# Kernel optimization log

Measured on AMD Instinct MI355X. Metric: run time of the kernel, lower is better.

## Reference

```python
import jax, jax.numpy as jnp
import numpy as np

D = 1024
H = 16
K = 32768
EPS = 1e-5


def setup_inputs() -> dict:
    key = jax.random.key(0)
    ks = jax.random.split(key, 12)
    s = 1.0 / np.sqrt(D)
    return {
        "query": jax.random.normal(ks[0], (D,), jnp.float32),
        "neighbors": jax.random.normal(ks[1], (K, D), jnp.float32),
        # nn.MultiheadAttention params
        "in_proj_w": jax.random.uniform(ks[2], (3 * D, D), jnp.float32, -s, s),
        "in_proj_b": jnp.zeros((3 * D,), jnp.float32),
        "out_proj_w": jax.random.uniform(ks[3], (D, D), jnp.float32, -s, s),
        "out_proj_b": jnp.zeros((D,), jnp.float32),
        # FFN params
        "w1": jax.random.uniform(ks[4], (4 * D, D), jnp.float32, -s, s),
        "b1": jnp.zeros((4 * D,), jnp.float32),
        "w2": jax.random.uniform(ks[5], (D, 4 * D), jnp.float32, -s, s),
        "b2": jnp.zeros((D,), jnp.float32),
        # LayerNorm params
        "g1": jnp.ones((D,), jnp.float32),
        "be1": jnp.zeros((D,), jnp.float32),
        "g2": jnp.ones((D,), jnp.float32),
        "be2": jnp.zeros((D,), jnp.float32),
    }


def _layernorm(x, g, b):
    m = jnp.mean(x, axis=-1, keepdims=True)
    v = jnp.var(x, axis=-1, keepdims=True)
    return (x - m) * jax.lax.rsqrt(v + EPS) * g + b


def reference(query, neighbors, in_proj_w, in_proj_b, out_proj_w, out_proj_b,
              w1, b1, w2, b2, g1, be1, g2, be2):
    dh = D // H
    wq, wk, wv = in_proj_w[:D], in_proj_w[D:2 * D], in_proj_w[2 * D:]
    bq, bk, bv = in_proj_b[:D], in_proj_b[D:2 * D], in_proj_b[2 * D:]

    q = (query @ wq.T + bq).reshape(H, dh)            # [H, dh]
    k = (neighbors @ wk.T + bk).reshape(K, H, dh)     # [K, H, dh]
    v = (neighbors @ wv.T + bv).reshape(K, H, dh)

    scores = jnp.einsum('hd,khd->hk', q, k) / np.sqrt(dh)  # [H, K]
    attn = jax.nn.softmax(scores, axis=-1)
    ctx = jnp.einsum('hk,khd->hd', attn, v).reshape(D)      # [D]
    attn_out = ctx @ out_proj_w.T + out_proj_b

    x = _layernorm(query + attn_out, g1, be1)
    ffn = jax.nn.gelu(x @ w1.T + b1, approximate=False) @ w2.T + b2
    return _layernorm(x + ffn, g2, be2)
```

## Files before the change

### kernel.cpp

```cpp
#include <hip/hip_runtime.h>
#include <hip/hip_bf16.h>

#define D 1024
#define H 16
#define DH 64
#define KN 32768
#define EPS 1e-5f

__device__ __forceinline__ float wave_sum(float v){
  #pragma unroll
  for (int off = 32; off; off >>= 1) v += __shfl_xor(v, off, 64);
  return v;
}

#define GLL(gp, lp) __builtin_amdgcn_global_load_lds((const __attribute__((address_space(1))) void*)(gp), (__attribute__((address_space(3))) void*)(lp), 16, 0, 0)

__global__ void g_qproj(const float* __restrict__ query, const float* __restrict__ ipw,
                        const float* __restrict__ ipb, float* __restrict__ q){
  int j = blockIdx.x, l = threadIdx.x;
  const float4* qv = (const float4*)(query + l*16);
  const float4* wv = (const float4*)(ipw + (size_t)j*D + l*16);
  float acc = 0.f;
  #pragma unroll
  for (int t = 0; t < 4; t++){
    float4 a = qv[t], b = wv[t];
    acc += a.x*b.x + a.y*b.y + a.z*b.z + a.w*b.w;
  }
  acc = wave_sum(acc);
  if (l == 0) q[j] = acc + ipb[j];
}

__global__ __launch_bounds__(256) void g_qk(const float* __restrict__ ipw, const float* __restrict__ ipb,
                                            const float* __restrict__ q, float* __restrict__ qk,
                                            float* __restrict__ sb){
  int b = blockIdx.x, t = threadIdx.x;
  int h = b >> 2, sl = b & 3;
  int jg = t >> 6, c = t & 63;
  __shared__ float qh[DH];
  __shared__ float4 red[256];
  if (t < DH) qh[t] = q[h*DH + t];
  __syncthreads();
  if (t < DH){
    float p = qh[t] * ipb[D + h*DH + t];
    p = wave_sum(p);
    if (t == 0 && sl == 0) sb[h] = p;
  }
  float4 acc = make_float4(0.f,0.f,0.f,0.f);
  for (int jj = 0; jj < 16; jj++){
    int j = jg*16 + jj;
    float4 w = *((const float4*)(ipw + (size_t)(D + h*DH + j)*D) + sl*64 + c);
    float qj = qh[j];
    acc.x += qj*w.x; acc.y += qj*w.y; acc.z += qj*w.z; acc.w += qj*w.w;
  }
  red[t] = acc;
  __syncthreads();
  if (jg == 0){
    float4 a = red[c], b1 = red[64+c], c1 = red[128+c], d1 = red[192+c];
    float4 r = make_float4(a.x+b1.x+c1.x+d1.x, a.y+b1.y+c1.y+d1.y,
                           a.z+b1.z+c1.z+d1.z, a.w+b1.w+c1.w+d1.w);
    ((float4*)(qk + h*D))[sl*64 + c] = r;
  }
}

__global__ __launch_bounds__(256, 2) void g_attn(const float* __restrict__ nbr, const float* __restrict__ qk,
                       const float* __restrict__ sb, float* __restrict__ lpart,
                       float* __restrict__ part, int rows_per_blk){
  __shared__ __align__(16) float tile[2][8*D];
  const int t = threadIdx.x;
  const int w = t >> 6, ci = t & 63;
  const int wb = t & ~63;
  const int g = (ci >> 4) & 3;
  const float sbl = sb[w*4 + g];

  float qk0[16], qk1[16], qk2[16], qk3[16];
  {
    const float4* p0 = (const float4*)(qk + (w*4+0)*D);
    const float4* p1 = (const float4*)(qk + (w*4+1)*D);
    const float4* p2 = (const float4*)(qk + (w*4+2)*D);
    const float4* p3 = (const float4*)(qk + (w*4+3)*D);
    #pragma unroll
    for (int c = 0; c < 4; c++){
      float4 f;
      f = p0[c*64 + ci]; qk0[4*c]=f.x; qk0[4*c+1]=f.y; qk0[4*c+2]=f.z; qk0[4*c+3]=f.w;
      f = p1[c*64 + ci]; qk1[4*c]=f.x; qk1[4*c+1]=f.y; qk1[4*c+2]=f.z; qk1[4*c+3]=f.w;
      f = p2[c*64 + ci]; qk2[4*c]=f.x; qk2[4*c+1]=f.y; qk2[4*c+2]=f.z; qk2[4*c+3]=f.w;
      f = p3[c*64 + ci]; qk3[4*c]=f.x; qk3[4*c+1]=f.y; qk3[4*c+2]=f.z; qk3[4*c+3]=f.w;
    }
  }
  float acc0[16], acc1[16], acc2[16], acc3[16];
  #pragma unroll
  for (int i = 0; i < 16; i++){ acc0[i]=0.f; acc1[i]=0.f; acc2[i]=0.f; acc3[i]=0.f; }
  float lsum = 0.f;

  const int k0 = blockIdx.x * rows_per_blk;
  const int ntiles = rows_per_blk >> 3;
  const uint4* gb = (const uint4*)nbr;

  {
    const uint4* gsrc = gb + (size_t)k0*256;
    #pragma unroll
    for (int i = 0; i < 8; i++) GLL(gsrc + i*256 + t, &tile[0][(i*256 + wb)*4]);
  }
  __syncthreads();

  #pragma unroll 1
  for (int tl = 0; tl < ntiles; tl++){
    int cur = tl & 1;
    if (tl + 1 < ntiles){
      const uint4* gsrc = gb + (size_t)(k0 + (tl+1)*8)*256;
      #pragma unroll
      for (int i = 0; i < 8; i++) GLL(gsrc + i*256 + t, &tile[cur^1][(i*256 + wb)*4]);
    }
    #pragma unroll 1
    for (int r = 0; r < 8; r++){
      const float4* row4 = (const float4*)(tile[cur]) + r*256;
      float xf[16];
      float s0=0.f, s1=0.f, s2=0.f, s3=0.f;
      #pragma unroll
      for (int c = 0; c < 4; c++){
        float4 a = row4[c*64 + ci];
        xf[4*c]=a.x; xf[4*c+1]=a.y; xf[4*c+2]=a.z; xf[4*c+3]=a.w;
        s0 += a.x*qk0[4*c] + a.y*qk0[4*c+1] + a.z*qk0[4*c+2] + a.w*qk0[4*c+3];
        s1 += a.x*qk1[4*c] + a.y*qk1[4*c+1] + a.z*qk1[4*c+2] + a.w*qk1[4*c+3];
        s2 += a.x*qk2[4*c] + a.y*qk2[4*c+1] + a.z*qk2[4*c+2] + a.w*qk2[4*c+3];
        s3 += a.x*qk3[4*c] + a.y*qk3[4*c+1] + a.z*qk3[4*c+2] + a.w*qk3[4*c+3];
      }
      const bool lo32 = (ci & 32) == 0;
      float za = lo32 ? s2 : s0;
      float ka = lo32 ? s0 : s2;
      float u02 = ka + __shfl_xor(za, 32, 64);
      float zb = lo32 ? s3 : s1;
      float kb = lo32 ? s1 : s3;
      float u13 = kb + __shfl_xor(zb, 32, 64);
      const bool lo16 = (ci & 16) == 0;
      float zc = lo16 ? u13 : u02;
      float kc = lo16 ? u02 : u13;
      float v = kc + __shfl_xor(zc, 16, 64);
      v += __shfl_xor(v, 8, 64);
      v += __shfl_xor(v, 4, 64);
      v += __shfl_xor(v, 2, 64);
      v += __shfl_xor(v, 1, 64);
      float pv = __expf((v + sbl)*0.125f);
      lsum += pv;
      float p0 = __shfl(pv, 0, 64);
      float p1 = __shfl(pv, 16, 64);
      float p2 = __shfl(pv, 32, 64);
      float p3 = __shfl(pv, 48, 64);
      #pragma unroll
      for (int j = 0; j < 16; j++){
        acc0[j] += p0*xf[j];
        acc1[j] += p1*xf[j];
        acc2[j] += p2*xf[j];
        acc3[j] += p3*xf[j];
      }
    }
    __syncthreads();
  }

  if ((ci & 15) == 0) lpart[blockIdx.x*H + w*4 + g] = lsum;
  float4* o = (float4*)(part + (size_t)blockIdx.x*(H*D) + (size_t)(w*4)*D);
  #pragma unroll
  for (int c = 0; c < 4; c++){
    o[0*256 + c*64 + ci] = make_float4(acc0[4*c], acc0[4*c+1], acc0[4*c+2], acc0[4*c+3]);
    o[1*256 + c*64 + ci] = make_float4(acc1[4*c], acc1[4*c+1], acc1[4*c+2], acc1[4*c+3]);
    o[2*256 + c*64 + ci] = make_float4(acc2[4*c], acc2[4*c+1], acc2[4*c+2], acc2[4*c+3]);
    o[3*256 + c*64 + ci] = make_float4(acc3[4*c], acc3[4*c+1], acc3[4*c+2], acc3[4*c+3]);
  }
}

__global__ __launch_bounds__(256) void g_red(const float* __restrict__ part, const float* __restrict__ lpart,
                                             float* __restrict__ nb, float* __restrict__ lh, int nblk){
  int b = blockIdx.x, t = threadIdx.x;
  __shared__ float red[256];
  if (b == 256){
    int h = t & 15, cs = t >> 4;
    int per = nblk >> 4;
    float s = 0.f;
    for (int k = 0; k < per; k++) s += lpart[(cs*per + k)*H + h];
    red[t] = s;
    __syncthreads();
    if (t < 16){
      float a = 0.f;
      #pragma unroll
      for (int i = 0; i < 16; i++) a += red[i*16 + t];
      lh[t] = a;
    }
    return;
  }
  int o0 = b * 64;
  int oo = t & 63, cs = t >> 6;
  int per = nblk >> 2;
  float s = 0.f;
  #pragma unroll 8
  for (int k = 0; k < per; k++) s += part[(size_t)(cs*per + k)*(H*D) + o0 + oo];
  red[t] = s;
  __syncthreads();
  if (t < 64) nb[o0 + t] = red[t] + red[64+t] + red[128+t] + red[192+t];
}

__global__ void g_ctx(const float* __restrict__ ipw, const float* __restrict__ ipb,
                      const float* __restrict__ nb, const float* __restrict__ lh,
                      float* __restrict__ ctx){
  int j = blockIdx.x, l = threadIdx.x, h = j >> 6;
  const float4* wv = (const float4*)(ipw + (size_t)(2*D + j)*D + l*16);
  const float4* nv = (const float4*)(nb + h*D + l*16);
  float acc = 0.f;
  #pragma unroll
  for (int t = 0; t < 4; t++){
    float4 b = wv[t], n = nv[t];
    acc += b.x*n.x + b.y*n.y + b.z*n.z + b.w*n.w;
  }
  acc = wave_sum(acc);
  if (l == 0) ctx[j] = acc/lh[h] + ipb[2*D + j];
}

__global__ void g_attnout(const float* __restrict__ opw, const float* __restrict__ opb,
                          const float* __restrict__ query, const float* __restrict__ ctx,
                          float* __restrict__ xb){
  int j = blockIdx.x, l = threadIdx.x;
  const float4* wv = (const float4*)(opw + (size_t)j*D + l*16);
  const float4* cv = (const float4*)(ctx + l*16);
  float acc = 0.f;
  #pragma unroll
  for (int t = 0; t < 4; t++){
    float4 b = wv[t], c = cv[t];
    acc += b.x*c.x + b.y*c.y + b.z*c.z + b.w*c.w;
  }
  acc = wave_sum(acc);
  if (l == 0) xb[j] = query[j] + acc + opb[j];
}

__global__ __launch_bounds__(256) void g_ffn1(const float* __restrict__ w1, const float* __restrict__ b1,
                                              const float* __restrict__ xb,
                                              const float* __restrict__ g1, const float* __restrict__ be1,
                                              float* __restrict__ xln, float* __restrict__ h1){
  int t = threadIdx.x, b = blockIdx.x;
  __shared__ float xs[D];
  __shared__ float red[8];
  float4 v = ((const float4*)xb)[t];
  float s = wave_sum(v.x + v.y + v.z + v.w);
  if ((t & 63) == 0) red[t >> 6] = s;
  __syncthreads();
  float m = (red[0]+red[1]+red[2]+red[3]) * (1.0f/D);
  float4 d = make_float4(v.x-m, v.y-m, v.z-m, v.w-m);
  float s2 = wave_sum(d.x*d.x + d.y*d.y + d.z*d.z + d.w*d.w);
  if ((t & 63) == 0) red[4 + (t >> 6)] = s2;
  __syncthreads();
  float var = (red[4]+red[5]+red[6]+red[7]) * (1.0f/D);
  float rs = rsqrtf(var + EPS);
  float4 gg = ((const float4*)g1)[t], bb = ((const float4*)be1)[t];
  float4 r = make_float4(d.x*rs*gg.x + bb.x, d.y*rs*gg.y + bb.y,
                         d.z*rs*gg.z + bb.z, d.w*rs*gg.w + bb.w);
  ((float4*)xs)[t] = r;
  if (b == 0) ((float4*)xln)[t] = r;
  __syncthreads();

  int w = t >> 6, l = t & 63;
  const float4* xs4 = (const float4*)xs;
  #pragma unroll 1
  for (int rr = 0; rr < 4; rr++){
    int j = b*16 + w*4 + rr;
    const float4* wr = (const float4*)(w1 + (size_t)j*D);
    float a = 0.f;
    #pragma unroll
    for (int c = 0; c < 4; c++){
      float4 ww = wr[c*64 + l], xx = xs4[c*64 + l];
      a += ww.x*xx.x + ww.y*xx.y + ww.z*xx.z + ww.w*xx.w;
    }
    a = wave_sum(a);
    if (l == 0){
      float z = a + b1[j];
      h1[j] = 0.5f*z*(1.0f + erff(z*0.70710678118654752f));
    }
  }
}

__global__ void g_ffn2(const float* __restrict__ w2, const float* __restrict__ b2v,
                       const float* __restrict__ h1, float* __restrict__ y){
  int j = blockIdx.x, l = threadIdx.x;
  const float4* wv = (const float4*)(w2 + (size_t)j*4096 + l*64);
  const float4* hv = (const float4*)(h1 + l*64);
  float acc = 0.f;
  #pragma unroll
  for (int t = 0; t < 16; t++){
    float4 b = wv[t], hh = hv[t];
    acc += b.x*hh.x + b.y*hh.y + b.z*hh.z + b.w*hh.w;
  }
  acc = wave_sum(acc);
  if (l == 0) y[j] = acc + b2v[j];
}

__global__ __launch_bounds__(1024) void g_ln2(const float* __restrict__ xln, const float* __restrict__ y,
                                              const float* __restrict__ g, const float* __restrict__ be,
                                              float* __restrict__ out){
  int t = threadIdx.x;
  __shared__ float red[16];
  __shared__ float bc;
  float v = xln[t] + y[t];
  float s = wave_sum(v);
  if ((t & 63) == 0) red[t >> 6] = s;
  __syncthreads();
  if (t == 0){ float a = 0.f; for (int i = 0; i < 16; i++) a += red[i]; bc = a*(1.0f/D); }
  __syncthreads();
  float m = bc;
  float d = v - m;
  float s2 = wave_sum(d*d);
  if ((t & 63) == 0) red[t >> 6] = s2;
  __syncthreads();
  if (t == 0){ float a = 0.f; for (int i = 0; i < 16; i++) a += red[i]; bc = a*(1.0f/D); }
  __syncthreads();
  float rs = rsqrtf(bc + EPS);
  out[t] = d*rs*g[t] + be[t];
}

extern "C" void kernel_launch(void* const* d_in, const int* in_sizes, int n_in,
                              void* d_out, int out_size, void* d_ws, size_t ws_size,
                              hipStream_t stream) {
  const float* query = (const float*)d_in[0];
  const float* nbr   = (const float*)d_in[1];
  const float* ipw   = (const float*)d_in[2];
  const float* ipb   = (const float*)d_in[3];
  const float* opw   = (const float*)d_in[4];
  const float* opb   = (const float*)d_in[5];
  const float* w1    = (const float*)d_in[6];
  const float* b1    = (const float*)d_in[7];
  const float* w2    = (const float*)d_in[8];
  const float* b2v   = (const float*)d_in[9];
  const float* g1    = (const float*)d_in[10];
  const float* be1   = (const float*)d_in[11];
  const float* g2    = (const float*)d_in[12];
  const float* be2   = (const float*)d_in[13];

  float* ws    = (float*)d_ws;
  float* q     = ws;
  float* qk    = q + D;
  float* sb    = qk + H*D;
  float* lh    = sb + 16;
  float* ctx   = lh + 16;
  float* xb    = ctx + D;
  float* xln   = xb + D;
  float* h1    = xln + D;
  float* y     = h1 + 4*D;
  float* nb    = y + D;
  float* lpart = nb + H*D;
  float* part  = lpart + 8192;

  size_t fixed_bytes = (size_t)(part - ws) * 4;
  int nblk = 512;
  while (nblk > 64 && fixed_bytes + (size_t)nblk*H*D*4 > ws_size) nblk >>= 1;
  int rows_per_blk = KN / nblk;

  g_qproj  <<<1024, 64, 0, stream>>>(query, ipw, ipb, q);
  g_qk     <<<64, 256, 0, stream>>>(ipw, ipb, q, qk, sb);
  g_attn   <<<nblk, 256, 0, stream>>>(nbr, qk, sb, lpart, part, rows_per_blk);
  g_red    <<<257, 256, 0, stream>>>(part, lpart, nb, lh, nblk);
  g_ctx    <<<1024, 64, 0, stream>>>(ipw, ipb, nb, lh, ctx);
  g_attnout<<<1024, 64, 0, stream>>>(opw, opb, query, ctx, xb);
  g_ffn1   <<<256, 256, 0, stream>>>(w1, b1, xb, g1, be1, xln, h1);
  g_ffn2   <<<1024, 64, 0, stream>>>(w2, b2v, h1, y);
  g_ln2    <<<1, 1024, 0, stream>>>(xln, y, g2, be2, (float*)d_out);
}
```

Baseline: 299.4 us.

## Fuse tail stages into one persistent kernel with grid barriers; pair rows in attention

```diff
diff --git a/kernel.cpp b/kernel.cpp
--- a/kernel.cpp
+++ b/kernel.cpp
@@ -13,33 +13,54 @@
   return v;
 }
 
+__device__ __forceinline__ void gbar(unsigned int* bar, unsigned int target){
+  __syncthreads();
+  if (threadIdx.x == 0){
+    __threadfence();
+    atomicAdd(bar, 1u);
+    while (__hip_atomic_load(bar, __ATOMIC_RELAXED, __HIP_MEMORY_SCOPE_AGENT) < target){
+      __builtin_amdgcn_s_sleep(2);
+    }
+  }
+  __syncthreads();
+  __threadfence();
+}
+
 #define GLL(gp, lp) __builtin_amdgcn_global_load_lds((const __attribute__((address_space(1))) void*)(gp), (__attribute__((address_space(3))) void*)(lp), 16, 0, 0)
 
-__global__ void g_qproj(const float* __restrict__ query, const float* __restrict__ ipw,
-                        const float* __restrict__ ipb, float* __restrict__ q){
-  int j = blockIdx.x, l = threadIdx.x;
-  const float4* qv = (const float4*)(query + l*16);
-  const float4* wv = (const float4*)(ipw + (size_t)j*D + l*16);
-  float acc = 0.f;
-  #pragma unroll
-  for (int t = 0; t < 4; t++){
-    float4 a = qv[t], b = wv[t];
-    acc += a.x*b.x + a.y*b.y + a.z*b.z + a.w*b.w;
-  }
-  acc = wave_sum(acc);
-  if (l == 0) q[j] = acc + ipb[j];
-}
-
-__global__ __launch_bounds__(256) void g_qk(const float* __restrict__ ipw, const float* __restrict__ ipb,
-                                            const float* __restrict__ q, float* __restrict__ qk,
-                                            float* __restrict__ sb){
+__global__ __launch_bounds__(256) void g_qk(const float* __restrict__ query,
+                                            const float* __restrict__ ipw, const float* __restrict__ ipb,
+                                            float* __restrict__ qk, float* __restrict__ sb,
+                                            unsigned int* __restrict__ bar){
   int b = blockIdx.x, t = threadIdx.x;
   int h = b >> 2, sl = b & 3;
-  int jg = t >> 6, c = t & 63;
+  int w = t >> 6, ci = t & 63;
   __shared__ float qh[DH];
   __shared__ float4 red[256];
-  if (t < DH) qh[t] = q[h*DH + t];
-  __syncthreads();
+  if (b == 0 && t == 0) *bar = 0u;
+
+  {
+    int cq = ci & 15, rq = ci >> 4;
+    const float4* qv = (const float4*)query;
+    #pragma unroll
+    for (int b4 = 0; b4 < 4; b4++){
+      int jr = w*16 + b4*4 + rq;
+      const float4* wr = (const float4*)(ipw + (size_t)(h*DH + jr)*D);
+      float a = 0.f;
+      #pragma unroll
+      for (int c = 0; c < 4; c++){
+        float4 ww = wr[c*16 + cq], qq = qv[c*16 + cq];
+        a += ww.x*qq.x + ww.y*qq.y + ww.z*qq.z + ww.w*qq.w;
+      }
+      a += __shfl_xor(a, 1, 64);
+      a += __shfl_xor(a, 2, 64);
+      a += __shfl_xor(a, 4, 64);
+      a += __shfl_xor(a, 8, 64);
+      if (cq == 0) qh[jr] = a + ipb[h*DH + jr];
+    }
+  }
+  __syncthreads();
+
   if (t < DH){
     float p = qh[t] * ipb[D + h*DH + t];
     p = wave_sum(p);
@@ -47,19 +68,38 @@
   }
   float4 acc = make_float4(0.f,0.f,0.f,0.f);
   for (int jj = 0; jj < 16; jj++){
-    int j = jg*16 + jj;
-    float4 w = *((const float4*)(ipw + (size_t)(D + h*DH + j)*D) + sl*64 + c);
+    int j = w*16 + jj;
+    float4 ww = *((const float4*)(ipw + (size_t)(D + h*DH + j)*D) + sl*64 + ci);
     float qj = qh[j];
-    acc.x += qj*w.x; acc.y += qj*w.y; acc.z += qj*w.z; acc.w += qj*w.w;
+    acc.x += qj*ww.x; acc.y += qj*ww.y; acc.z += qj*ww.z; acc.w += qj*ww.w;
   }
   red[t] = acc;
   __syncthreads();
-  if (jg == 0){
-    float4 a = red[c], b1 = red[64+c], c1 = red[128+c], d1 = red[192+c];
+  if (w == 0){
+    float4 a = red[ci], b1 = red[64+ci], c1 = red[128+ci], d1 = red[192+ci];
     float4 r = make_float4(a.x+b1.x+c1.x+d1.x, a.y+b1.y+c1.y+d1.y,
                            a.z+b1.z+c1.z+d1.z, a.w+b1.w+c1.w+d1.w);
-    ((float4*)(qk + h*D))[sl*64 + c] = r;
-  }
+    ((float4*)(qk + h*D))[sl*64 + ci] = r;
+  }
+}
+
+__device__ __forceinline__ float bf4(float s0, float s1, float s2, float s3, int ci){
+  const bool lo32 = (ci & 32) == 0;
+  float za = lo32 ? s2 : s0;
+  float ka = lo32 ? s0 : s2;
+  float u02 = ka + __shfl_xor(za, 32, 64);
+  float zb = lo32 ? s3 : s1;
+  float kb = lo32 ? s1 : s3;
+  float u13 = kb + __shfl_xor(zb, 32, 64);
+  const bool lo16 = (ci & 16) == 0;
+  float zc = lo16 ? u13 : u02;
+  float kc = lo16 ? u02 : u13;
+  float v = kc + __shfl_xor(zc, 16, 64);
+  v += __shfl_xor(v, 8, 64);
+  v += __shfl_xor(v, 4, 64);
+  v += __shfl_xor(v, 2, 64);
+  v += __shfl_xor(v, 1, 64);
+  return v;
 }
 
 __global__ __launch_bounds__(256, 2) void g_attn(const float* __restrict__ nbr, const float* __restrict__ qk,
@@ -111,49 +151,49 @@
       #pragma unroll
       for (int i = 0; i < 8; i++) GLL(gsrc + i*256 + t, &tile[cur^1][(i*256 + wb)*4]);
     }
+    __builtin_amdgcn_s_setprio(1);
     #pragma unroll 1
-    for (int r = 0; r < 8; r++){
-      const float4* row4 = (const float4*)(tile[cur]) + r*256;
-      float xf[16];
-      float s0=0.f, s1=0.f, s2=0.f, s3=0.f;
+    for (int r = 0; r < 8; r += 2){
+      const float4* rowA = (const float4*)(tile[cur]) + r*256;
+      float xfA[16], xfB[16];
+      float sA0=0.f,sA1=0.f,sA2=0.f,sA3=0.f;
+      float sB0=0.f,sB1=0.f,sB2=0.f,sB3=0.f;
       #pragma unroll
       for (int c = 0; c < 4; c++){
-        float4 a = row4[c*64 + ci];
-        xf[4*c]=a.x; xf[4*c+1]=a.y; xf[4*c+2]=a.z; xf[4*c+3]=a.w;
-        s0 += a.x*qk0[4*c] + a.y*qk0[4*c+1] + a.z*qk0[4*c+2] + a.w*qk0[4*c+3];
-        s1 += a.x*qk1[4*c] + a.y*qk1[4*c+1] + a.z*qk1[4*c+2] + a.w*qk1[4*c+3];
-        s2 += a.x*qk2[4*c] + a.y*qk2[4*c+1] + a.z*qk2[4*c+2] + a.w*qk2[4*c+3];
-        s3 += a.x*qk3[4*c] + a.y*qk3[4*c+1] + a.z*qk3[4*c+2] + a.w*qk3[4*c+3];
-      }
-      const bool lo32 = (ci & 32) == 0;
-      float za = lo32 ? s2 : s0;
-      float ka = lo32 ? s0 : s2;
-      float u02 = ka + __shfl_xor(za, 32, 64);
-      float zb = lo32 ? s3 : s1;
-      float kb = lo32 ? s1 : s3;
-      float u13 = kb + __shfl_xor(zb, 32, 64);
-      const bool lo16 = (ci & 16) == 0;
-      float zc = lo16 ? u13 : u02;
-      float kc = lo16 ? u02 : u13;
-      float v = kc + __shfl_xor(zc, 16, 64);
-      v += __shfl_xor(v, 8, 64);
-      v += __shfl_xor(v, 4, 64);
-      v += __shfl_xor(v, 2, 64);
-      v += __shfl_xor(v, 1, 64);
-      float pv = __expf((v + sbl)*0.125f);
-      lsum += pv;
-      float p0 = __shfl(pv, 0, 64);
-      float p1 = __shfl(pv, 16, 64);
-      float p2 = __shfl(pv, 32, 64);
-      float p3 = __shfl(pv, 48, 64);
+        float4 a = rowA[c*64 + ci];
+        xfA[4*c]=a.x; xfA[4*c+1]=a.y; xfA[4*c+2]=a.z; xfA[4*c+3]=a.w;
+        sA0 += a.x*qk0[4*c] + a.y*qk0[4*c+1] + a.z*qk0[4*c+2] + a.w*qk0[4*c+3];
+        sA1 += a.x*qk1[4*c] + a.y*qk1[4*c+1] + a.z*qk1[4*c+2] + a.w*qk1[4*c+3];
+        sA2 += a.x*qk2[4*c] + a.y*qk2[4*c+1] + a.z*qk2[4*c+2] + a.w*qk2[4*c+3];
+        sA3 += a.x*qk3[4*c] + a.y*qk3[4*c+1] + a.z*qk3[4*c+2] + a.w*qk3[4*c+3];
+      }
+      #pragma unroll
+      for (int c = 0; c < 4; c++){
+        float4 a = rowA[256 + c*64 + ci];
+        xfB[4*c]=a.x; xfB[4*c+1]=a.y; xfB[4*c+2]=a.z; xfB[4*c+3]=a.w;
+        sB0 += a.x*qk0[4*c] + a.y*qk0[4*c+1] + a.z*qk0[4*c+2] + a.w*qk0[4*c+3];
+        sB1 += a.x*qk1[4*c] + a.y*qk1[4*c+1] + a.z*qk1[4*c+2] + a.w*qk1[4*c+3];
+        sB2 += a.x*qk2[4*c] + a.y*qk2[4*c+1] + a.z*qk2[4*c+2] + a.w*qk2[4*c+3];
+        sB3 += a.x*qk3[4*c] + a.y*qk3[4*c+1] + a.z*qk3[4*c+2] + a.w*qk3[4*c+3];
+      }
+      float vA = bf4(sA0, sA1, sA2, sA3, ci);
+      float vB = bf4(sB0, sB1, sB2, sB3, ci);
+      float pA = __expf((vA + sbl)*0.125f);
+      float pB = __expf((vB + sbl)*0.125f);
+      lsum += pA + pB;
+      float pA0 = __shfl(pA, 0, 64), pA1 = __shfl(pA, 16, 64);
+      float pA2 = __shfl(pA, 32, 64), pA3 = __shfl(pA, 48, 64);
+      float pB0 = __shfl(pB, 0, 64), pB1 = __shfl(pB, 16, 64);
+      float pB2 = __shfl(pB, 32, 64), pB3 = __shfl(pB, 48, 64);
       #pragma unroll
       for (int j = 0; j < 16; j++){
-        acc0[j] += p0*xf[j];
-        acc1[j] += p1*xf[j];
-        acc2[j] += p2*xf[j];
-        acc3[j] += p3*xf[j];
-      }
-    }
+        acc0[j] += pA0*xfA[j] + pB0*xfB[j];
+        acc1[j] += pA1*xfA[j] + pB1*xfB[j];
+        acc2[j] += pA2*xfA[j] + pB2*xfB[j];
+        acc3[j] += pA3*xfA[j] + pB3*xfB[j];
+      }
+    }
+    __builtin_amdgcn_s_setprio(0);
     __syncthreads();
   }
 
@@ -168,149 +208,150 @@
   }
 }
 
-__global__ __launch_bounds__(256) void g_red(const float* __restrict__ part, const float* __restrict__ lpart,
-                                             float* __restrict__ nb, float* __restrict__ lh, int nblk){
-  int b = blockIdx.x, t = threadIdx.x;
+__global__ __launch_bounds__(256) void g_tail(
+    const float* __restrict__ part, const float* __restrict__ lpart,
+    const float* __restrict__ ipw, const float* __restrict__ ipb,
+    const float* __restrict__ opw, const float* __restrict__ opb,
+    const float* __restrict__ query,
+    const float* __restrict__ w1, const float* __restrict__ b1,
+    const float* __restrict__ w2, const float* __restrict__ b2v,
+    const float* __restrict__ g1, const float* __restrict__ be1,
+    const float* __restrict__ g2, const float* __restrict__ be2,
+    float* __restrict__ nb, float* __restrict__ lh,
+    float* __restrict__ ctx, float* __restrict__ xb,
+    float* __restrict__ h1, float* __restrict__ y,
+    float* __restrict__ out, unsigned int* __restrict__ bar, int nblk){
+  const int b = blockIdx.x, t = threadIdx.x;
+  const int w = t >> 6, l = t & 63;
+  __shared__ __align__(16) float xs[D];
   __shared__ float red[256];
-  if (b == 256){
-    int h = t & 15, cs = t >> 4;
-    int per = nblk >> 4;
+
+  {
+    int o0 = b*64;
+    int per = nblk >> 2;
     float s = 0.f;
-    for (int k = 0; k < per; k++) s += lpart[(cs*per + k)*H + h];
+    #pragma unroll 8
+    for (int k = 0; k < per; k++) s += part[(size_t)(w*per + k)*(H*D) + o0 + l];
     red[t] = s;
     __syncthreads();
-    if (t < 16){
+    if (t < 64) nb[o0 + t] = red[t] + red[64+t] + red[128+t] + red[192+t];
+    if (b == 0){
+      __syncthreads();
+      int hh = t & 15, cs2 = t >> 4, per2 = nblk >> 4;
+      float s2 = 0.f;
+      for (int k = 0; k < per2; k++) s2 += lpart[(cs2*per2 + k)*H + hh];
+      red[t] = s2;
+      __syncthreads();
+      if (t < 16){
+        float a = 0.f;
+        #pragma unroll
+        for (int i = 0; i < 16; i++) a += red[i*16 + t];
+        lh[t] = a;
+      }
+    }
+  }
+  gbar(bar, 256);
+
+  {
+    int j = b*4 + w, hh = j >> 6;
+    const float4* wv = (const float4*)(ipw + (size_t)(2*D + j)*D + l*16);
+    const float4* nv = (const float4*)(nb + hh*D + l*16);
+    float acc = 0.f;
+    #pragma unroll
+    for (int c = 0; c < 4; c++){
+      float4 bb = wv[c], nn = nv[c];
+      acc += bb.x*nn.x + bb.y*nn.y + bb.z*nn.z + bb.w*nn.w;
+    }
+    acc = wave_sum(acc);
+    if (l == 0) ctx[j] = acc/lh[hh] + ipb[2*D + j];
+  }
+  gbar(bar, 512);
+
+  {
+    int j = b*4 + w;
+    const float4* wv = (const float4*)(opw + (size_t)j*D + l*16);
+    const float4* cv = (const float4*)(ctx + l*16);
+    float acc = 0.f;
+    #pragma unroll
+    for (int c = 0; c < 4; c++){
+      float4 bb = wv[c], cc = cv[c];
+      acc += bb.x*cc.x + bb.y*cc.y + bb.z*cc.z + bb.w*cc.w;
+    }
+    acc = wave_sum(acc);
+    if (l == 0) xb[j] = query[j] + acc + opb[j];
+  }
+  gbar(bar, 768);
+
+  {
+    float4 v = ((const float4*)xb)[t];
+    float s = wave_sum(v.x + v.y + v.z + v.w);
+    if (l == 0) red[w] = s;
+    __syncthreads();
+    float m = (red[0]+red[1]+red[2]+red[3]) * (1.0f/D);
+    float4 dd = make_float4(v.x-m, v.y-m, v.z-m, v.w-m);
+    float s2 = wave_sum(dd.x*dd.x + dd.y*dd.y + dd.z*dd.z + dd.w*dd.w);
+    if (l == 0) red[4 + w] = s2;
+    __syncthreads();
+    float var = (red[4]+red[5]+red[6]+red[7]) * (1.0f/D);
+    float rs = rsqrtf(var + EPS);
+    float4 gg = ((const float4*)g1)[t], bb = ((const float4*)be1)[t];
+    float4 r = make_float4(dd.x*rs*gg.x + bb.x, dd.y*rs*gg.y + bb.y,
+                           dd.z*rs*gg.z + bb.z, dd.w*rs*gg.w + bb.w);
+    ((float4*)xs)[t] = r;
+    __syncthreads();
+    const float4* xs4 = (const float4*)xs;
+    #pragma unroll 1
+    for (int rr = 0; rr < 4; rr++){
+      int j = b*16 + w*4 + rr;
+      const float4* wr = (const float4*)(w1 + (size_t)j*D);
       float a = 0.f;
       #pragma unroll
-      for (int i = 0; i < 16; i++) a += red[i*16 + t];
-      lh[t] = a;
-    }
-    return;
-  }
-  int o0 = b * 64;
-  int oo = t & 63, cs = t >> 6;
-  int per = nblk >> 2;
-  float s = 0.f;
-  #pragma unroll 8
-  for (int k = 0; k < per; k++) s += part[(size_t)(cs*per + k)*(H*D) + o0 + oo];
-  red[t] = s;
-  __syncthreads();
-  if (t < 64) nb[o0 + t] = red[t] + red[64+t] + red[128+t] + red[192+t];
-}
-
-__global__ void g_ctx(const float* __restrict__ ipw, const float* __restrict__ ipb,
-                      const float* __restrict__ nb, const float* __restrict__ lh,
-                      float* __restrict__ ctx){
-  int j = blockIdx.x, l = threadIdx.x, h = j >> 6;
-  const float4* wv = (const float4*)(ipw + (size_t)(2*D + j)*D + l*16);
-  const float4* nv = (const float4*)(nb + h*D + l*16);
-  float acc = 0.f;
-  #pragma unroll
-  for (int t = 0; t < 4; t++){
-    float4 b = wv[t], n = nv[t];
-    acc += b.x*n.x + b.y*n.y + b.z*n.z + b.w*n.w;
-  }
-  acc = wave_sum(acc);
-  if (l == 0) ctx[j] = acc/lh[h] + ipb[2*D + j];
-}
-
-__global__ void g_attnout(const float* __restrict__ opw, const float* __restrict__ opb,
-                          const float* __restrict__ query, const float* __restrict__ ctx,
-                          float* __restrict__ xb){
-  int j = blockIdx.x, l = threadIdx.x;
-  const float4* wv = (const float4*)(opw + (size_t)j*D + l*16);
-  const float4* cv = (const float4*)(ctx + l*16);
-  float acc = 0.f;
-  #pragma unroll
-  for (int t = 0; t < 4; t++){
-    float4 b = wv[t], c = cv[t];
-    acc += b.x*c.x + b.y*c.y + b.z*c.z + b.w*c.w;
-  }
-  acc = wave_sum(acc);
-  if (l == 0) xb[j] = query[j] + acc + opb[j];
-}
-
-__global__ __launch_bounds__(256) void g_ffn1(const float* __restrict__ w1, const float* __restrict__ b1,
-                                              const float* __restrict__ xb,
-                                              const float* __restrict__ g1, const float* __restrict__ be1,
-                                              float* __restrict__ xln, float* __restrict__ h1){
-  int t = threadIdx.x, b = blockIdx.x;
-  __shared__ float xs[D];
-  __shared__ float red[8];
-  float4 v = ((const float4*)xb)[t];
-  float s = wave_sum(v.x + v.y + v.z + v.w);
-  if ((t & 63) == 0) red[t >> 6] = s;
-  __syncthreads();
-  float m = (red[0]+red[1]+red[2]+red[3]) * (1.0f/D);
-  float4 d = make_float4(v.x-m, v.y-m, v.z-m, v.w-m);
-  float s2 = wave_sum(d.x*d.x + d.y*d.y + d.z*d.z + d.w*d.w);
-  if ((t & 63) == 0) red[4 + (t >> 6)] = s2;
-  __syncthreads();
-  float var = (red[4]+red[5]+red[6]+red[7]) * (1.0f/D);
-  float rs = rsqrtf(var + EPS);
-  float4 gg = ((const float4*)g1)[t], bb = ((const float4*)be1)[t];
-  float4 r = make_float4(d.x*rs*gg.x + bb.x, d.y*rs*gg.y + bb.y,
-                         d.z*rs*gg.z + bb.z, d.w*rs*gg.w + bb.w);
-  ((float4*)xs)[t] = r;
-  if (b == 0) ((float4*)xln)[t] = r;
-  __syncthreads();
-
-  int w = t >> 6, l = t & 63;
-  const float4* xs4 = (const float4*)xs;
-  #pragma unroll 1
-  for (int rr = 0; rr < 4; rr++){
-    int j = b*16 + w*4 + rr;
-    const float4* wr = (const float4*)(w1 + (size_t)j*D);
-    float a = 0.f;
-    #pragma unroll
-    for (int c = 0; c < 4; c++){
-      float4 ww = wr[c*64 + l], xx = xs4[c*64 + l];
-      a += ww.x*xx.x + ww.y*xx.y + ww.z*xx.z + ww.w*xx.w;
-    }
-    a = wave_sum(a);
-    if (l == 0){
-      float z = a + b1[j];
-      h1[j] = 0.5f*z*(1.0f + erff(z*0.70710678118654752f));
-    }
-  }
-}
-
-__global__ void g_ffn2(const float* __restrict__ w2, const float* __restrict__ b2v,
-                       const float* __restrict__ h1, float* __restrict__ y){
-  int j = blockIdx.x, l = threadIdx.x;
-  const float4* wv = (const float4*)(w2 + (size_t)j*4096 + l*64);
-  const float4* hv = (const float4*)(h1 + l*64);
-  float acc = 0.f;
-  #pragma unroll
-  for (int t = 0; t < 16; t++){
-    float4 b = wv[t], hh = hv[t];
-    acc += b.x*hh.x + b.y*hh.y + b.z*hh.z + b.w*hh.w;
-  }
-  acc = wave_sum(acc);
-  if (l == 0) y[j] = acc + b2v[j];
-}
-
-__global__ __launch_bounds__(1024) void g_ln2(const float* __restrict__ xln, const float* __restrict__ y,
-                                              const float* __restrict__ g, const float* __restrict__ be,
-                                              float* __restrict__ out){
-  int t = threadIdx.x;
-  __shared__ float red[16];
-  __shared__ float bc;
-  float v = xln[t] + y[t];
-  float s = wave_sum(v);
-  if ((t & 63) == 0) red[t >> 6] = s;
-  __syncthreads();
-  if (t == 0){ float a = 0.f; for (int i = 0; i < 16; i++) a += red[i]; bc = a*(1.0f/D); }
-  __syncthreads();
-  float m = bc;
-  float d = v - m;
-  float s2 = wave_sum(d*d);
-  if ((t & 63) == 0) red[t >> 6] = s2;
-  __syncthreads();
-  if (t == 0){ float a = 0.f; for (int i = 0; i < 16; i++) a += red[i]; bc = a*(1.0f/D); }
-  __syncthreads();
-  float rs = rsqrtf(bc + EPS);
-  out[t] = d*rs*g[t] + be[t];
+      for (int c = 0; c < 4; c++){
+        float4 ww = wr[c*64 + l], xx = xs4[c*64 + l];
+        a += ww.x*xx.x + ww.y*xx.y + ww.z*xx.z + ww.w*xx.w;
+      }
+      a = wave_sum(a);
+      if (l == 0){
+        float z = a + b1[j];
+        h1[j] = 0.5f*z*(1.0f + erff(z*0.70710678118654752f));
+      }
+    }
+  }
+  gbar(bar, 1024);
+
+  {
+    int j = b*4 + w;
+    const float4* wv = (const float4*)(w2 + (size_t)j*4096 + l*64);
+    const float4* hv = (const float4*)(h1 + l*64);
+    float acc = 0.f;
+    #pragma unroll
+    for (int c = 0; c < 16; c++){
+      float4 bb = wv[c], hh2 = hv[c];
+      acc += bb.x*hh2.x + bb.y*hh2.y + bb.z*hh2.z + bb.w*hh2.w;
+    }
+    acc = wave_sum(acc);
+    if (l == 0) y[j] = acc + b2v[j];
+  }
+  gbar(bar, 1280);
+
+  if (b == 0){
+    float4 xv = ((const float4*)xs)[t];
+    float4 yv = ((const float4*)y)[t];
+    float4 v = make_float4(xv.x+yv.x, xv.y+yv.y, xv.z+yv.z, xv.w+yv.w);
+    float s = wave_sum(v.x + v.y + v.z + v.w);
+    if (l == 0) red[w] = s;
+    __syncthreads();
+    float m = (red[0]+red[1]+red[2]+red[3]) * (1.0f/D);
+    float4 dd = make_float4(v.x-m, v.y-m, v.z-m, v.w-m);
+    float s2 = wave_sum(dd.x*dd.x + dd.y*dd.y + dd.z*dd.z + dd.w*dd.w);
+    if (l == 0) red[4 + w] = s2;
+    __syncthreads();
+    float var = (red[4]+red[5]+red[6]+red[7]) * (1.0f/D);
+    float rs = rsqrtf(var + EPS);
+    float4 gg = ((const float4*)g2)[t], bb = ((const float4*)be2)[t];
+    ((float4*)out)[t] = make_float4(dd.x*rs*gg.x + bb.x, dd.y*rs*gg.y + bb.y,
+                                    dd.z*rs*gg.z + bb.z, dd.w*rs*gg.w + bb.w);
+  }
 }
 
 extern "C" void kernel_launch(void* const* d_in, const int* in_sizes, int n_in,
@@ -332,17 +373,16 @@
   const float* be2   = (const float*)d_in[13];
 
   float* ws    = (float*)d_ws;
-  float* q     = ws;
-  float* qk    = q + D;
+  float* qk    = ws;
   float* sb    = qk + H*D;
   float* lh    = sb + 16;
   float* ctx   = lh + 16;
   float* xb    = ctx + D;
-  float* xln   = xb + D;
-  float* h1    = xln + D;
+  float* h1    = xb + D;
   float* y     = h1 + 4*D;
   float* nb    = y + D;
-  float* lpart = nb + H*D;
+  unsigned int* bar = (unsigned int*)(nb + H*D);
+  float* lpart = nb + H*D + 16;
   float* part  = lpart + 8192;
 
   size_t fixed_bytes = (size_t)(part - ws) * 4;
@@ -350,13 +390,9 @@
   while (nblk > 64 && fixed_bytes + (size_t)nblk*H*D*4 > ws_size) nblk >>= 1;
   int rows_per_blk = KN / nblk;
 
-  g_qproj  <<<1024, 64, 0, stream>>>(query, ipw, ipb, q);
-  g_qk     <<<64, 256, 0, stream>>>(ipw, ipb, q, qk, sb);
-  g_attn   <<<nblk, 256, 0, stream>>>(nbr, qk, sb, lpart, part, rows_per_blk);
-  g_red    <<<257, 256, 0, stream>>>(part, lpart, nb, lh, nblk);
-  g_ctx    <<<1024, 64, 0, stream>>>(ipw, ipb, nb, lh, ctx);
-  g_attnout<<<1024, 64, 0, stream>>>(opw, opb, query, ctx, xb);
-  g_ffn1   <<<256, 256, 0, stream>>>(w1, b1, xb, g1, be1, xln, h1);
-  g_ffn2   <<<1024, 64, 0, stream>>>(w2, b2v, h1, y);
-  g_ln2    <<<1, 1024, 0, stream>>>(xln, y, g2, be2, (float*)d_out);
-}
+  g_qk  <<<64, 256, 0, stream>>>(query, ipw, ipb, qk, sb, bar);
+  g_attn<<<nblk, 256, 0, stream>>>(nbr, qk, sb, lpart, part, rows_per_blk);
+  g_tail<<<256, 256, 0, stream>>>(part, lpart, ipw, ipb, opw, opb, query,
+                                  w1, b1, w2, b2v, g1, be1, g2, be2,
+                                  nb, lh, ctx, xb, h1, y, (float*)d_out, bar, nblk);
+}
```

New measurement: 433.0 us. 1.45x slower.
